# Kernel optimization log

Hardware: AMD Instinct MI355X
Metric: run time of the kernel (lower is better)

The kernel has to match this reference:

```python
import jax, jax.numpy as jnp
import numpy as np
from jax import lax

B, H, W, CIN = 32, 64, 64, 128
F, KH, KW = 256, 3, 3
NCLS = 10


def setup_inputs() -> dict:
    key = jax.random.key(0)
    k1, k2, k3, k4 = jax.random.split(key, 4)
    x = jax.random.normal(k1, (B, H, W, CIN), dtype=jnp.float32)
    classes = jax.random.randint(k2, (B, 1), 0, NCLS, dtype=jnp.int32)
    kernel = jax.random.normal(k3, (NCLS, KH, KW, CIN, F), dtype=jnp.float32) * 0.05
    bias = jax.random.normal(k4, (NCLS, F), dtype=jnp.float32) * 0.05
    return {"x": x, "classes": classes, "kernel": kernel, "bias": bias}


def reference(x, classes, kernel, bias):
    # classes: [B,1] -> [B]
    cls = jnp.squeeze(classes, axis=1)
    k_per = kernel[cls]   # [B, KH, KW, CIN, F] per-sample gathered expert kernel
    b_per = bias[cls]     # [B, F]

    def conv_one(xi, ki):
        # xi: [H,W,CIN], ki: [KH,KW,CIN,F]
        y = lax.conv_general_dilated(
            xi[None], ki,
            window_strides=(1, 1),
            padding="SAME",
            rhs_dilation=(1, 1),
            dimension_numbers=("NHWC", "HWIO", "NHWC"),
        )
        return y[0]

    out = jax.vmap(conv_one)(x, k_per)          # [B,H,W,F]
    out = out + b_per[:, None, None, :]
    return out
```

## Files before the change

kernel.cpp:

```cpp
#include <hip/hip_runtime.h>
#include <stdint.h>

#define BATCH 32
#define CINX 128
#define FOUT 256
#define NCLS 10
#define NSTEP 18

typedef __bf16 bf16x8 __attribute__((ext_vector_type(8)));
typedef float f32x4 __attribute__((ext_vector_type(4)));

#define WT_SLAB 32768
#define WT_BYTES ((size_t)NCLS * 9 * WT_SLAB * 2)
#define Z_BYTES 4096
#define X16_BYTES ((size_t)BATCH * 4096 * CINX * 2)
#define WS_NEED (WT_BYTES + Z_BYTES + X16_BYTES)

#define BAR() __builtin_amdgcn_s_barrier()
#define VMW4() asm volatile("s_waitcnt vmcnt(4)" ::: "memory")
#define VMW0() asm volatile("s_waitcnt vmcnt(0)" ::: "memory")

__device__ __forceinline__ void gl16(const __bf16* g, __bf16* l) {
    __builtin_amdgcn_global_load_lds(
        (const __attribute__((address_space(1))) void*)g,
        (__attribute__((address_space(3))) void*)l, 16, 0, 0);
}

__global__ __launch_bounds__(256) void prep_w8(const float* __restrict__ kin,
                                               __bf16* __restrict__ wt) {
    __shared__ __bf16 tile[128 * 260];
    const int slab = blockIdx.x;
    const float* src = kin + (size_t)slab * (CINX * FOUT);
    __bf16* dst = wt + (size_t)slab * WT_SLAB;
    const int t = threadIdx.x;
#pragma unroll
    for (int i = 0; i < 32; ++i) {
        int e4 = t + i * 256;
        int c = e4 >> 6, f4 = e4 & 63;
        f32x4 v = *(const f32x4*)(src + (size_t)e4 * 4);
        __bf16* p = &tile[c * 260 + f4 * 4];
        p[0] = (__bf16)v[0]; p[1] = (__bf16)v[1];
        p[2] = (__bf16)v[2]; p[3] = (__bf16)v[3];
    }
    __syncthreads();
#pragma unroll
    for (int i = 0; i < 16; ++i) {
        int g = t + i * 256;
        int h = g >> 10;
        int u = g & 1023;
        int f = u >> 2, slot = u & 3;
        int cu = slot ^ ((f >> 1) & 3);
        int c0 = h * 32 + cu * 8;
        bf16x8 o;
#pragma unroll
        for (int j = 0; j < 8; ++j) o[j] = tile[(c0 + j) * 260 + f];
        *(bf16x8*)(dst + (size_t)g * 8) = o;
    }
}

__global__ __launch_bounds__(256) void prep_x(const float* __restrict__ x,
                                              __bf16* __restrict__ x16,
                                              __bf16* __restrict__ zbuf) {
    const size_t u = (size_t)blockIdx.x * 256 + threadIdx.x;
    f32x4 a = *(const f32x4*)(x + u * 8);
    f32x4 c = *(const f32x4*)(x + u * 8 + 4);
    bf16x8 o;
#pragma unroll
    for (int j = 0; j < 4; ++j) { o[j] = (__bf16)a[j]; o[4 + j] = (__bf16)c[j]; }
    *(bf16x8*)(x16 + u * 8) = o;
    if (blockIdx.x == 0 && threadIdx.x < 128) {
        bf16x8 z;
#pragma unroll
        for (int j = 0; j < 8; ++j) z[j] = (__bf16)0.f;
        *(bf16x8*)(zbuf + (size_t)threadIdx.x * 8) = z;
    }
}

__global__ __launch_bounds__(512, 2) void conv_main8(
    const __bf16* __restrict__ xg16, const int* __restrict__ cls_g,
    const __bf16* __restrict__ wt, const float* __restrict__ bias,
    const __bf16* __restrict__ zbuf, float* __restrict__ out) {
    __shared__ __align__(16) __bf16 ldsA[2][2][1024 * 8];
    __shared__ __align__(16) __bf16 ldsB[2][2][1024 * 8];

    const int bid0 = blockIdx.x;
    const int swz  = (bid0 & 7) * 64 + (bid0 >> 3);
    const int b    = swz >> 4;
    const int pt   = swz & 15;
    const int cls  = cls_g[b];
    const int y0   = pt << 2;

    const int tid  = threadIdx.x;
    const int lane = tid & 63;
    const int wid  = tid >> 6;
    const int wm   = wid >> 2;
    const int wn   = wid & 3;
    const int l15  = lane & 15;
    const int l4   = lane >> 4;

    const __bf16* xb   = xg16 + (size_t)b * 4096 * CINX;
    const __bf16* wcls = wt + (size_t)cls * 9 * WT_SLAB;

    int pyA[2], gxA[2], cuoffA[2], uS[2];
#pragma unroll
    for (int i = 0; i < 2; ++i) {
        int u = i * 512 + tid;
        int px = u >> 2, slot = u & 3;
        uS[i] = u;
        pyA[i] = px >> 6;
        gxA[i] = px & 63;
        cuoffA[i] = (slot ^ ((px >> 1) & 3)) * 8;
    }
    int unA[8], unB[4];
#pragma unroll
    for (int mt = 0; mt < 8; ++mt) {
        int px = wm * 128 + mt * 16 + l15;
        unA[mt] = px * 4 + (l4 ^ ((px >> 1) & 3));
    }
#pragma unroll
    for (int nt = 0; nt < 4; ++nt) {
        int f = wn * 64 + nt * 16 + l15;
        unB[nt] = f * 4 + (l4 ^ ((f >> 1) & 3));
    }

    f32x4 acc[8][4];
#pragma unroll
    for (int i = 0; i < 8; ++i)
#pragma unroll
        for (int j = 0; j < 4; ++j)
#pragma unroll
            for (int r = 0; r < 4; ++r) acc[i][j][r] = 0.f;

    auto stage = [&](int s2, int kk) {
        const int p = s2 & 1;
        const int tap = s2 >> 1;
        const int dy = tap / 3 - 1, dx = tap % 3 - 1;
        const int choff = (s2 & 1) * 64 + kk * 32;
#pragma unroll
        for (int i = 0; i < 2; ++i) {
            const int gy = y0 + pyA[i] + dy;
            const int gx = gxA[i] + dx;
            const bool v = ((unsigned)gy < 64u) && ((unsigned)gx < 64u);
            const __bf16* src = v
                ? (xb + ((size_t)(gy * 64 + gx)) * CINX + choff + cuoffA[i])
                : (zbuf + (size_t)(uS[i] & 63) * 8);
            gl16(src, &ldsA[p][kk][(size_t)uS[i] * 8]);
        }
        const __bf16* wsrc = wcls + (size_t)tap * WT_SLAB +
                             (size_t)((s2 & 1) * 2 + kk) * 8192;
#pragma unroll
        for (int i = 0; i < 2; ++i)
            gl16(wsrc + (size_t)uS[i] * 8, &ldsB[p][kk][(size_t)uS[i] * 8]);
    };

    bf16x8 afr[4], bfr[4];
    auto ldB = [&](int p, int kk) {
#pragma unroll
        for (int nt = 0; nt < 4; ++nt)
            bfr[nt] = *(const bf16x8*)&ldsB[p][kk][(size_t)unB[nt] * 8];
    };
    auto ldA = [&](int p, int kk, int mh) {
#pragma unroll
        for (int mt = 0; mt < 4; ++mt)
            afr[mt] = *(const bf16x8*)&ldsA[p][kk][(size_t)unA[mh * 4 + mt] * 8];
    };
    auto mm = [&](int mh) {
        __builtin_amdgcn_s_setprio(1);
#pragma unroll
        for (int mt = 0; mt < 4; ++mt)
#pragma unroll
            for (int nt = 0; nt < 4; ++nt)
                acc[mh * 4 + mt][nt] = __builtin_amdgcn_mfma_f32_16x16x32_bf16(
                    afr[mt], bfr[nt], acc[mh * 4 + mt][nt], 0, 0, 0);
        __builtin_amdgcn_s_setprio(0);
    };

    stage(0, 0);
    stage(0, 1);
    VMW4();
    BAR();

    for (int s = 0; s < NSTEP - 1; ++s) {
        const int p = s & 1;
        ldB(p, 0); ldA(p, 0, 0); stage(s + 1, 0);
        BAR(); mm(0); BAR();
        ldA(p, 0, 1);
        VMW4();
        BAR(); mm(1); BAR();
        ldB(p, 1); ldA(p, 1, 0); stage(s + 1, 1);
        BAR(); mm(0); BAR();
        ldA(p, 1, 1);
        VMW4();
        BAR(); mm(1); BAR();
    }
    ldB(1, 0); ldA(1, 0, 0);
    BAR(); mm(0); BAR();
    ldA(1, 0, 1);
    VMW0();
    BAR(); mm(1); BAR();
    ldB(1, 1); ldA(1, 1, 0);
    BAR(); mm(0); BAR();
    ldA(1, 1, 1);
    mm(1);

    float bv[4];
#pragma unroll
    for (int nt = 0; nt < 4; ++nt)
        bv[nt] = bias[cls * FOUT + wn * 64 + nt * 16 + l15];

    float* ob = out + ((size_t)b * 4096 + (size_t)pt * 256) * FOUT;
#pragma unroll
    for (int mt = 0; mt < 8; ++mt) {
#pragma unroll
        for (int r = 0; r < 4; ++r) {
            const int row = wm * 128 + mt * 16 + l4 * 4 + r;
            float* orow = ob + (size_t)row * FOUT;
#pragma unroll
            for (int nt = 0; nt < 4; ++nt)
                orow[wn * 64 + nt * 16 + l15] = acc[mt][nt][r] + bv[nt];
        }
    }
}

__global__ __launch_bounds__(256) void prep_w_fb(const float* __restrict__ kin,
                                                 __bf16* __restrict__ wt) {
    __shared__ __bf16 tile[128 * 260];
    const int slab = blockIdx.x;
    const float* src = kin + (size_t)slab * (CINX * FOUT);
    __bf16* dst = wt + (size_t)slab * (16 * 256 * 8);
    const int t = threadIdx.x;
#pragma unroll
    for (int i = 0; i < 32; ++i) {
        int e4 = t + i * 256;
        int c = e4 >> 6, f4 = e4 & 63;
        f32x4 v = *(const f32x4*)(src + (size_t)e4 * 4);
        __bf16* p = &tile[c * 260 + f4 * 4];
        p[0] = (__bf16)v[0]; p[1] = (__bf16)v[1];
        p[2] = (__bf16)v[2]; p[3] = (__bf16)v[3];
    }
    __syncthreads();
#pragma unroll
    for (int i = 0; i < 16; ++i) {
        int g = t + i * 256;
        int cu = g >> 8, f = g & 255;
        bf16x8 o;
#pragma unroll
        for (int j = 0; j < 8; ++j) o[j] = tile[(cu * 8 + j) * 260 + f];
        *(bf16x8*)(dst + (size_t)g * 8) = o;
    }
}

__global__ __launch_bounds__(512, 2) void conv_fb(
    const float* __restrict__ xg, const int* __restrict__ cls_g,
    const __bf16* __restrict__ wt, const float* __restrict__ bias,
    float* __restrict__ out) {
    __shared__ __align__(16) __bf16 ldsA[2][8 * 256 * 8];
    __shared__ __align__(16) __bf16 ldsB[2][8 * 256 * 8];
    const int bid0 = blockIdx.x;
    const int swz = (bid0 & 7) * 64 + (bid0 >> 3);
    const int b = swz >> 4, pt = swz & 15;
    const int cls = cls_g[b];
    const int y0 = pt << 2;
    const int tid = threadIdx.x, lane = tid & 63, wid = tid >> 6;
    const int wm = wid >> 2, wn = wid & 3, l15 = lane & 15, l4 = lane >> 4;
    const float* xb = xg + (size_t)b * 4096 * CINX;
    const __bf16* wcls = wt + (size_t)cls * 9 * (16 * 256 * 8);
    const int tpx = tid >> 1, tch = (tid & 1) * 32;
    const int py = tpx >> 6, px_ = tpx & 63;
    f32x4 acc[8][4];
#pragma unroll
    for (int i = 0; i < 8; ++i)
#pragma unroll
        for (int j = 0; j < 4; ++j)
#pragma unroll
            for (int r = 0; r < 4; ++r) acc[i][j][r] = 0.f;
    f32x4 va[8];
    auto issueB = [&](int s, int buf) {
        const int tap = s >> 1, chalf = (s & 1) << 6;
        const __bf16* wsrc = wcls + (size_t)tap * (16 * 256 * 8) + chalf * 256;
#pragma unroll
        for (int i = 0; i < 4; ++i) {
            const int u = i * 512 + tid;
            gl16(wsrc + (size_t)u * 8, &ldsB[buf][(size_t)u * 8]);
        }
    };
    auto issueA = [&](int s) {
        const int tap = s >> 1, chalf = (s & 1) << 6;
        const int dy = tap / 3 - 1, dx = tap % 3 - 1;
        const int gy = y0 + py + dy, gx = px_ + dx;
        const bool valid = ((unsigned)gy < 64u) && ((unsigned)gx < 64u);
        const float* src = xb + ((size_t)(gy * 64 + gx)) * CINX + chalf + tch;
        if (valid) {
#pragma unroll
            for (int j2 = 0; j2 < 8; ++j2) va[j2] = *(const f32x4*)(src + j2 * 4);
        } else {
#pragma unroll
            for (int j2 = 0; j2 < 8; ++j2)
#pragma unroll
                for (int q = 0; q < 4; ++q) va[j2][q] = 0.f;
        }
    };
    auto writeA = [&](int buf) {
#pragma unroll
        for (int j = 0; j < 4; ++j) {
            bf16x8 pk;
#pragma unroll
            for (int q = 0; q < 4; ++q) {
                pk[q] = (__bf16)va[2 * j][q];
                pk[4 + q] = (__bf16)va[2 * j + 1][q];
            }
            const int u = ((tid & 1) * 4 + j) * 256 + tpx;
            *(bf16x8*)(&ldsA[buf][(size_t)u * 8]) = pk;
        }
    };
    auto compute = [&](int buf) {
#pragma unroll
        for (int kk = 0; kk < 2; ++kk) {
            const int cu = kk * 4 + l4;
            bf16x8 afr[8], bfr[4];
#pragma unroll
            for (int mt = 0; mt < 8; ++mt)
                afr[mt] = *(const bf16x8*)(
                    &ldsA[buf][(size_t)(cu * 256 + wm * 128 + mt * 16 + l15) * 8]);
#pragma unroll
            for (int nt = 0; nt < 4; ++nt)
                bfr[nt] = *(const bf16x8*)(
                    &ldsB[buf][(size_t)(cu * 256 + wn * 64 + nt * 16 + l15) * 8]);
#pragma unroll
            for (int mt = 0; mt < 8; ++mt)
#pragma unroll
                for (int nt = 0; nt < 4; ++nt)
                    acc[mt][nt] = __builtin_amdgcn_mfma_f32_16x16x32_bf16(
                        afr[mt], bfr[nt], acc[mt][nt], 0, 0, 0);
        }
    };
    issueB(0, 0);
    issueA(0);
    writeA(0);
    __syncthreads();
    int cur = 0;
    for (int s = 0; s < NSTEP - 1; ++s) {
        issueB(s + 1, cur ^ 1);
        issueA(s + 1);
        compute(cur);
        writeA(cur ^ 1);
        __syncthreads();
        cur ^= 1;
    }
    compute(cur);
    float bv[4];
#pragma unroll
    for (int nt = 0; nt < 4; ++nt)
        bv[nt] = bias[cls * FOUT + wn * 64 + nt * 16 + l15];
    float* ob = out + ((size_t)b * 4096 + (size_t)pt * 256) * FOUT;
#pragma unroll
    for (int mt = 0; mt < 8; ++mt) {
#pragma unroll
        for (int r = 0; r < 4; ++r) {
            const int row = wm * 128 + mt * 16 + l4 * 4 + r;
            float* orow = ob + (size_t)row * FOUT;
#pragma unroll
            for (int nt = 0; nt < 4; ++nt)
                orow[wn * 64 + nt * 16 + l15] = acc[mt][nt][r] + bv[nt];
        }
    }
}

extern "C" void kernel_launch(void* const* d_in, const int* in_sizes, int n_in,
                              void* d_out, int out_size, void* d_ws, size_t ws_size,
                              hipStream_t stream) {
    const float* x       = (const float*)d_in[0];
    const int*   classes = (const int*)d_in[1];
    const float* kin     = (const float*)d_in[2];
    const float* bias    = (const float*)d_in[3];
    float* out = (float*)d_out;

    char* ws = (char*)d_ws;
    __bf16* wt   = (__bf16*)ws;
    __bf16* zbuf = (__bf16*)(ws + WT_BYTES);
    __bf16* x16  = (__bf16*)(ws + WT_BYTES + Z_BYTES);

    if (ws_size >= WS_NEED) {
        prep_w8<<<dim3(NCLS * 9), dim3(256), 0, stream>>>(kin, wt);
        prep_x<<<dim3(8192), dim3(256), 0, stream>>>(x, x16, zbuf);
        conv_main8<<<dim3(512), dim3(512), 0, stream>>>(x16, classes, wt, bias,
                                                        zbuf, out);
    } else {
        prep_w_fb<<<dim3(NCLS * 9), dim3(256), 0, stream>>>(kin, wt);
        conv_fb<<<dim3(512), dim3(512), 0, stream>>>(x, classes, wt, bias, out);
    }
}
```

Baseline: 108.9 us.

## Merge prep kernels into one launch and cut redundant barriers in conv main loop

The weight-conversion and input-conversion kernels are merged into a single launch that branches on block index, saving one kernel launch and letting both run concurrently. In the main conv loop most workgroup barriers around the MFMA phases are removed, leaving one barrier per half-step after the vmcnt wait, with sched_barrier added to stop the compiler from moving code across it. This cuts barrier stalls, but it risks LDS read/write races between the async global_load_lds staging and the fragment reads, since fewer barriers now order double-buffer reuse.

```diff
diff --git a/kernel.cpp b/kernel.cpp
--- a/kernel.cpp
+++ b/kernel.cpp
@@ -17,6 +17,7 @@
 #define WS_NEED (WT_BYTES + Z_BYTES + X16_BYTES)
 
 #define BAR() __builtin_amdgcn_s_barrier()
+#define SCHEDBAR() __builtin_amdgcn_sched_barrier(0)
 #define VMW4() asm volatile("s_waitcnt vmcnt(4)" ::: "memory")
 #define VMW0() asm volatile("s_waitcnt vmcnt(0)" ::: "memory")
 
@@ -26,53 +27,55 @@
         (__attribute__((address_space(3))) void*)l, 16, 0, 0);
 }
 
-__global__ __launch_bounds__(256) void prep_w8(const float* __restrict__ kin,
-                                               __bf16* __restrict__ wt) {
-    __shared__ __bf16 tile[128 * 260];
-    const int slab = blockIdx.x;
-    const float* src = kin + (size_t)slab * (CINX * FOUT);
-    __bf16* dst = wt + (size_t)slab * WT_SLAB;
-    const int t = threadIdx.x;
-#pragma unroll
-    for (int i = 0; i < 32; ++i) {
-        int e4 = t + i * 256;
-        int c = e4 >> 6, f4 = e4 & 63;
-        f32x4 v = *(const f32x4*)(src + (size_t)e4 * 4);
-        __bf16* p = &tile[c * 260 + f4 * 4];
-        p[0] = (__bf16)v[0]; p[1] = (__bf16)v[1];
-        p[2] = (__bf16)v[2]; p[3] = (__bf16)v[3];
-    }
-    __syncthreads();
-#pragma unroll
-    for (int i = 0; i < 16; ++i) {
-        int g = t + i * 256;
-        int h = g >> 10;
-        int u = g & 1023;
-        int f = u >> 2, slot = u & 3;
-        int cu = slot ^ ((f >> 1) & 3);
-        int c0 = h * 32 + cu * 8;
+__global__ __launch_bounds__(256) void prep_all(const float* __restrict__ kin,
+                                                __bf16* __restrict__ wt,
+                                                const float* __restrict__ x,
+                                                __bf16* __restrict__ x16,
+                                                __bf16* __restrict__ zbuf) {
+    if (blockIdx.x < NCLS * 9) {
+        __shared__ __bf16 tile[128 * 260];
+        const int slab = blockIdx.x;
+        const float* src = kin + (size_t)slab * (CINX * FOUT);
+        __bf16* dst = wt + (size_t)slab * WT_SLAB;
+        const int t = threadIdx.x;
+#pragma unroll
+        for (int i = 0; i < 32; ++i) {
+            int e4 = t + i * 256;
+            int c = e4 >> 6, f4 = e4 & 63;
+            f32x4 v = *(const f32x4*)(src + (size_t)e4 * 4);
+            __bf16* p = &tile[c * 260 + f4 * 4];
+            p[0] = (__bf16)v[0]; p[1] = (__bf16)v[1];
+            p[2] = (__bf16)v[2]; p[3] = (__bf16)v[3];
+        }
+        __syncthreads();
+#pragma unroll
+        for (int i = 0; i < 16; ++i) {
+            int g = t + i * 256;
+            int h = g >> 10;
+            int u = g & 1023;
+            int f = u >> 2, slot = u & 3;
+            int cu = slot ^ ((f >> 1) & 3);
+            int c0 = h * 32 + cu * 8;
+            bf16x8 o;
+#pragma unroll
+            for (int j = 0; j < 8; ++j) o[j] = tile[(c0 + j) * 260 + f];
+            *(bf16x8*)(dst + (size_t)g * 8) = o;
+        }
+    } else {
+        const int bx = blockIdx.x - NCLS * 9;
+        const size_t u = (size_t)bx * 256 + threadIdx.x;
+        f32x4 a = *(const f32x4*)(x + u * 8);
+        f32x4 c = *(const f32x4*)(x + u * 8 + 4);
         bf16x8 o;
 #pragma unroll
-        for (int j = 0; j < 8; ++j) o[j] = tile[(c0 + j) * 260 + f];
-        *(bf16x8*)(dst + (size_t)g * 8) = o;
-    }
-}
-
-__global__ __launch_bounds__(256) void prep_x(const float* __restrict__ x,
-                                              __bf16* __restrict__ x16,
-                                              __bf16* __restrict__ zbuf) {
-    const size_t u = (size_t)blockIdx.x * 256 + threadIdx.x;
-    f32x4 a = *(const f32x4*)(x + u * 8);
-    f32x4 c = *(const f32x4*)(x + u * 8 + 4);
-    bf16x8 o;
-#pragma unroll
-    for (int j = 0; j < 4; ++j) { o[j] = (__bf16)a[j]; o[4 + j] = (__bf16)c[j]; }
-    *(bf16x8*)(x16 + u * 8) = o;
-    if (blockIdx.x == 0 && threadIdx.x < 128) {
-        bf16x8 z;
-#pragma unroll
-        for (int j = 0; j < 8; ++j) z[j] = (__bf16)0.f;
-        *(bf16x8*)(zbuf + (size_t)threadIdx.x * 8) = z;
+        for (int j = 0; j < 4; ++j) { o[j] = (__bf16)a[j]; o[4 + j] = (__bf16)c[j]; }
+        *(bf16x8*)(x16 + u * 8) = o;
+        if (bx == 0 && threadIdx.x < 128) {
+            bf16x8 z;
+#pragma unroll
+            for (int j = 0; j < 8; ++j) z[j] = (__bf16)0.f;
+            *(bf16x8*)(zbuf + (size_t)threadIdx.x * 8) = z;
+        }
     }
 }
 
@@ -179,27 +182,34 @@
     stage(0, 1);
     VMW4();
     BAR();
+    SCHEDBAR();
 
     for (int s = 0; s < NSTEP - 1; ++s) {
         const int p = s & 1;
         ldB(p, 0); ldA(p, 0, 0); stage(s + 1, 0);
-        BAR(); mm(0); BAR();
+        mm(0);
         ldA(p, 0, 1);
         VMW4();
-        BAR(); mm(1); BAR();
+        BAR();
+        SCHEDBAR();
+        mm(1);
         ldB(p, 1); ldA(p, 1, 0); stage(s + 1, 1);
-        BAR(); mm(0); BAR();
+        mm(0);
         ldA(p, 1, 1);
         VMW4();
-        BAR(); mm(1); BAR();
+        BAR();
+        SCHEDBAR();
+        mm(1);
     }
     ldB(1, 0); ldA(1, 0, 0);
-    BAR(); mm(0); BAR();
+    mm(0);
     ldA(1, 0, 1);
     VMW0();
-    BAR(); mm(1); BAR();
+    BAR();
+    SCHEDBAR();
+    mm(1);
     ldB(1, 1); ldA(1, 1, 0);
-    BAR(); mm(0); BAR();
+    mm(0);
     ldA(1, 1, 1);
     mm(1);
 
@@ -381,8 +391,8 @@
     __bf16* x16  = (__bf16*)(ws + WT_BYTES + Z_BYTES);
 
     if (ws_size >= WS_NEED) {
-        prep_w8<<<dim3(NCLS * 9), dim3(256), 0, stream>>>(kin, wt);
-        prep_x<<<dim3(8192), dim3(256), 0, stream>>>(x, x16, zbuf);
+        prep_all<<<dim3(NCLS * 9 + 8192), dim3(256), 0, stream>>>(kin, wt, x,
+                                                                  x16, zbuf);
         conv_main8<<<dim3(512), dim3(512), 0, stream>>>(x16, classes, wt, bias,
                                                         zbuf, out);
     } else {
```

Result: faster. 101.7 us (-6.6%).
